# Performance work log

Hardware: AMD Instinct MI355X
Metric: run time of the kernel (lower is better)

The kernel has to match this reference:

```python
import jax, jax.numpy as jnp
import numpy as np

T, B, IN, H, OUT = 128, 128, 512, 512, 512


def _lstm_dir(x, W_ih, W_hh, b_ih, b_hh):
    # x: [T, B, IN]; W_ih: [4H, IN]; W_hh: [4H, H]; biases: [4H]
    # Precompute input contribution for all timesteps in one big GEMM.
    xw = jnp.einsum('tbi,gi->tbg', x, W_ih) + b_ih + b_hh  # [T, B, 4H]
    Hh = W_hh.shape[1]

    def step(carry, xw_t):
        h, c = carry
        gates = xw_t + h @ W_hh.T  # [B, 4H]
        i, f, g, o = jnp.split(gates, 4, axis=-1)  # PyTorch gate order i,f,g,o
        i = jax.nn.sigmoid(i)
        f = jax.nn.sigmoid(f)
        g = jnp.tanh(g)
        o = jax.nn.sigmoid(o)
        c = f * c + i * g
        h = o * jnp.tanh(c)
        return (h, c), h

    h0 = jnp.zeros((x.shape[1], Hh), x.dtype)
    c0 = jnp.zeros((x.shape[1], Hh), x.dtype)
    _, hs = jax.lax.scan(step, (h0, c0), xw)
    return hs  # [T, B, H]


def setup_inputs() -> dict:
    key = jax.random.key(0)
    ks = jax.random.split(key, 12)
    s_in = 1.0 / np.sqrt(H)
    u = lambda k, shape: jax.random.uniform(k, shape, jnp.float32, -s_in, s_in)
    return {
        'x': jax.random.normal(ks[0], (T, B, IN), jnp.float32),
        'W_ih_f': u(ks[1], (4 * H, IN)),
        'W_hh_f': u(ks[2], (4 * H, H)),
        'b_ih_f': u(ks[3], (4 * H,)),
        'b_hh_f': u(ks[4], (4 * H,)),
        'W_ih_b': u(ks[5], (4 * H, IN)),
        'W_hh_b': u(ks[6], (4 * H, H)),
        'b_ih_b': u(ks[7], (4 * H,)),
        'b_hh_b': u(ks[8], (4 * H,)),
        'W_lin': u(ks[9], (OUT, 2 * H)),
        'b_lin': u(ks[10], (OUT,)),
    }


def reference(x, W_ih_f, W_hh_f, b_ih_f, b_hh_f, W_ih_b, W_hh_b, b_ih_b, b_hh_b, W_lin, b_lin):
    h_fwd = _lstm_dir(x, W_ih_f, W_hh_f, b_ih_f, b_hh_f)                    # [T,B,H]
    h_bwd = _lstm_dir(x[::-1], W_ih_b, W_hh_b, b_ih_b, b_hh_b)[::-1]        # [T,B,H]
    out = jnp.concatenate([h_fwd, h_bwd], axis=-1)                          # [T,B,2H]
    out = jnp.einsum('tbh,oh->tbo', out, W_lin) + b_lin                     # [T,B,OUT]
    return out
```

## Files before the change

kernel.cpp:

```cpp
#include <hip/hip_runtime.h>

typedef unsigned short u16;
typedef unsigned long long u64;
typedef __attribute__((ext_vector_type(8))) short bf16x8;
typedef __attribute__((ext_vector_type(4))) float f32x4;

#define MFMA16(a, b, c) __builtin_amdgcn_mfma_f32_16x16x32_bf16((a), (b), (c), 0, 0, 0)

#define TT 128
#define BB 128
#define IN_ 512
#define HH 512
#define G4 2048
#define OUTD 512
#define TB 16384

#define AEXLD(p) __hip_atomic_load((p), __ATOMIC_RELAXED, __HIP_MEMORY_SCOPE_AGENT)

__device__ __forceinline__ u16 f2bf(float f) {
    union { float f; unsigned u; } v; v.f = f;
    unsigned r = v.u + 0x7FFFu + ((v.u >> 16) & 1u);
    return (u16)(r >> 16);
}
__device__ __forceinline__ float bf2f(u16 h) {
    union { unsigned u; float f; } v; v.u = ((unsigned)h) << 16; return v.f;
}
__device__ __forceinline__ float sigmoid_f(float x) { return 1.f / (1.f + __expf(-x)); }
__device__ __forceinline__ float tanh_f(float x) {
    float e = __expf(2.f * x);
    return 1.f - 2.f / (e + 1.f);
}

typedef unsigned __attribute__((address_space(1))) guint;
typedef unsigned __attribute__((address_space(3))) luint;
__device__ __forceinline__ void gll16(const u16* g, u16* l) {
    __builtin_amdgcn_global_load_lds((guint*)(void*)g, (luint*)(void*)l, 16, 0, 0);
}

__global__ void prep_kernel(
    const float* __restrict__ x,
    const float* __restrict__ Wihf, const float* __restrict__ Wihb,
    const float* __restrict__ Whhf, const float* __restrict__ Whhb,
    const float* __restrict__ Wlin,
    const float* __restrict__ bihf, const float* __restrict__ bhhf,
    const float* __restrict__ bihb, const float* __restrict__ bhhb,
    u16* __restrict__ x_bf, u16* __restrict__ wih_cat,
    u16* __restrict__ whhf_bf, u16* __restrict__ whhb_bf,
    u16* __restrict__ wlin_bf, float* __restrict__ bias_cat,
    uint4* __restrict__ exch) {
    const int i0 = blockIdx.x * blockDim.x + threadIdx.x;
    const int stride = gridDim.x * blockDim.x;
    #define CVT4(SRC, DST, N4, DOFF)                                        \
        for (int i = i0; i < (N4); i += stride) {                           \
            float4 v = ((const float4*)(SRC))[i];                           \
            ushort4 o;                                                      \
            o.x = f2bf(v.x); o.y = f2bf(v.y);                               \
            o.z = f2bf(v.z); o.w = f2bf(v.w);                               \
            ((ushort4*)(DST))[(DOFF) + i] = o;                              \
        }
    CVT4(x, x_bf, (TB * IN_) / 4, 0)
    CVT4(Wihf, wih_cat, (G4 * IN_) / 4, 0)
    CVT4(Wihb, wih_cat, (G4 * IN_) / 4, (G4 * IN_) / 4)
    CVT4(Whhf, whhf_bf, (G4 * HH) / 4, 0)
    CVT4(Whhb, whhb_bf, (G4 * HH) / 4, 0)
    CVT4(Wlin, wlin_bf, (OUTD * 2 * HH) / 4, 0)
    #undef CVT4
    for (int i = i0; i < G4; i += stride) {
        bias_cat[i]      = bihf[i] + bhhf[i];
        bias_cat[G4 + i] = bihb[i] + bhhb[i];
    }
    for (int i = i0; i < 65536; i += stride)
        exch[i] = uint4{0u, 0u, 0u, 0u};
}

__global__ __launch_bounds__(256) void gemm_bias_kernel(
    const u16* __restrict__ A, const u16* __restrict__ W,
    const float* __restrict__ bias, void* __restrict__ Cout,
    int M, int N, int K, int out_is_bf16) {
    __shared__ __align__(16) u16 lA[128 * 64];
    __shared__ __align__(16) u16 lB[128 * 64];
    const int tid = threadIdx.x;
    const int m0 = blockIdx.x * 128;
    const int n0 = blockIdx.y * 128;
    const int wave = tid >> 6, lane = tid & 63;
    const int wm = wave >> 1, wn = wave & 1;
    const int lrow = lane & 15, lq = lane >> 4;
    const int srow = lane >> 3, soff = (lane & 7) * 8;

    f32x4 acc[4][4] = {};

    for (int kc = 0; kc < K; kc += 64) {
        #pragma unroll
        for (int i = 0; i < 4; ++i) {
            int chunk = wave + i * 4;
            int row = chunk * 8 + srow;
            gll16(&A[(size_t)(m0 + row) * K + kc + soff], &lA[chunk * 512]);
            gll16(&W[(size_t)(n0 + row) * K + kc + soff], &lB[chunk * 512]);
        }
        __syncthreads();
        #pragma unroll
        for (int ks = 0; ks < 2; ++ks) {
            bf16x8 af[4], bfr[4];
            #pragma unroll
            for (int mf = 0; mf < 4; ++mf)
                af[mf] = *(const bf16x8*)(&lA[(wm * 64 + mf * 16 + lrow) * 64 + ks * 32 + lq * 8]);
            #pragma unroll
            for (int nf = 0; nf < 4; ++nf)
                bfr[nf] = *(const bf16x8*)(&lB[(wn * 64 + nf * 16 + lrow) * 64 + ks * 32 + lq * 8]);
            #pragma unroll
            for (int mf = 0; mf < 4; ++mf)
                #pragma unroll
                for (int nf = 0; nf < 4; ++nf)
                    acc[mf][nf] = MFMA16(af[mf], bfr[nf], acc[mf][nf]);
        }
        __syncthreads();
    }

    #pragma unroll
    for (int mf = 0; mf < 4; ++mf) {
        #pragma unroll
        for (int nf = 0; nf < 4; ++nf) {
            int row = m0 + wm * 64 + mf * 16 + lq * 4;
            int col = n0 + wn * 64 + nf * 16 + lrow;
            float bv = bias[col];
            f32x4 v = acc[mf][nf];
            #pragma unroll
            for (int r = 0; r < 4; ++r) {
                float val = v[r] + bv;
                if (out_is_bf16)
                    ((u16*)Cout)[(size_t)(row + r) * N + col] = f2bf(val);
                else
                    ((float*)Cout)[(size_t)(row + r) * N + col] = val;
            }
        }
    }
}

__global__ __launch_bounds__(256, 1) void lstm_persist_kernel(
    const u16* __restrict__ xw, const u16* __restrict__ whh_f,
    const u16* __restrict__ whh_b, u16* __restrict__ hcat,
    u64* __restrict__ exch) {
    const int bx = blockIdx.x;
    const int dir = bx >> 7;
    const int bt = (bx >> 4) & 7;
    const int jt = bx & 15;
    const u16* __restrict__ whh = dir ? whh_b : whh_f;
    const int b0 = bt * 16;
    const int j0 = jt * 32;

    __shared__ __align__(16) u16 lh[16 * 520];
    __shared__ float sgate[4][16][33];

    const int tid = threadIdx.x;
    const int wave = tid >> 6, lane = tid & 63;
    const int lrow = lane & 15, lq = lane >> 4;

    const u16* wrow = whh + ((size_t)wave * HH + j0) * HH;
    bf16x8 w0[16], w1[16];
    #pragma unroll
    for (int kc = 0; kc < 16; ++kc) {
        w0[kc] = *(const bf16x8*)(&wrow[(size_t)lrow * HH + kc * 32 + lq * 8]);
        w1[kc] = *(const bf16x8*)(&wrow[(size_t)(16 + lrow) * HH + kc * 32 + lq * 8]);
    }
    #pragma unroll
    for (int kc = 0; kc < 16; ++kc)
        asm volatile("" : "+v"(w0[kc]), "+v"(w1[kc]));

    const int bl = tid >> 4;
    const int jj = (tid & 15) * 2;
    float cr0 = 0.f, cr1 = 0.f;

    const size_t my_ex = ((size_t)dir * BB + b0 + bl) * 256 + (j0 >> 1) + (tid & 15);

    for (int s = 0; s < TT; ++s) {
        const int t = dir ? (TT - 1 - s) : s;

        const u16* xrow = xw + ((size_t)t * BB + b0 + bl) * (2 * G4) + dir * G4 + j0 + jj;
        unsigned xg[4];
        #pragma unroll
        for (int g = 0; g < 4; ++g)
            xg[g] = *(const unsigned*)(xrow + (size_t)g * HH);

        f32x4 acc0 = {}, acc1 = {}, acc0b = {}, acc1b = {};
        if (s > 0) {
            const int p = (s - 1) & 1;
            const u64* ex = exch + ((size_t)(p * 2 + dir) * BB + b0) * 256 + tid;
            const u64 expect = ((u64)(unsigned)s << 48) | ((u64)(unsigned)s << 16);
            u64 v[16];
            for (;;) {
                #pragma unroll
                for (int i = 0; i < 16; ++i)
                    v[i] = AEXLD(ex + (size_t)i * 256);
                bool ok = true;
                #pragma unroll
                for (int i = 0; i < 16; ++i)
                    ok &= ((v[i] & 0xFFFF0000FFFF0000ull) == expect);
                if (ok) break;
            }
            #pragma unroll
            for (int i = 0; i < 16; ++i)
                *(unsigned*)(&lh[i * 520 + tid * 2]) =
                    (unsigned)(v[i] & 0xffffu) | (unsigned)((v[i] >> 16) & 0xffff0000u);
            __syncthreads();

            #pragma unroll
            for (int kc = 0; kc < 16; kc += 2) {
                bf16x8 a0 = *(const bf16x8*)(&lh[lrow * 520 + kc * 32 + lq * 8]);
                bf16x8 a1 = *(const bf16x8*)(&lh[lrow * 520 + (kc + 1) * 32 + lq * 8]);
                acc0  = MFMA16(a0, w0[kc], acc0);
                acc1  = MFMA16(a0, w1[kc], acc1);
                acc0b = MFMA16(a1, w0[kc + 1], acc0b);
                acc1b = MFMA16(a1, w1[kc + 1], acc1b);
            }
            acc0 += acc0b;
            acc1 += acc1b;
        }

        #pragma unroll
        for (int r = 0; r < 4; ++r) {
            sgate[wave][lq * 4 + r][lrow]      = acc0[r];
            sgate[wave][lq * 4 + r][16 + lrow] = acc1[r];
        }
        __syncthreads();

        float gi0 = sgate[0][bl][jj]     + bf2f((u16)(xg[0] & 0xffffu));
        float gf0 = sgate[1][bl][jj]     + bf2f((u16)(xg[1] & 0xffffu));
        float gg0 = sgate[2][bl][jj]     + bf2f((u16)(xg[2] & 0xffffu));
        float go0 = sgate[3][bl][jj]     + bf2f((u16)(xg[3] & 0xffffu));
        float gi1 = sgate[0][bl][jj + 1] + bf2f((u16)(xg[0] >> 16));
        float gf1 = sgate[1][bl][jj + 1] + bf2f((u16)(xg[1] >> 16));
        float gg1 = sgate[2][bl][jj + 1] + bf2f((u16)(xg[2] >> 16));
        float go1 = sgate[3][bl][jj + 1] + bf2f((u16)(xg[3] >> 16));

        float c0 = sigmoid_f(gf0) * cr0 + sigmoid_f(gi0) * tanh_f(gg0);
        float c1 = sigmoid_f(gf1) * cr1 + sigmoid_f(gi1) * tanh_f(gg1);
        cr0 = c0; cr1 = c1;
        float h0 = sigmoid_f(go0) * tanh_f(c0);
        float h1 = sigmoid_f(go1) * tanh_f(c1);

        unsigned hb0 = (unsigned)f2bf(h0), hb1 = (unsigned)f2bf(h1);
        unsigned tagv = (unsigned)(s + 1) << 16;
        u64 pv = (u64)(tagv | hb0) | ((u64)(tagv | hb1) << 32);
        __hip_atomic_store(exch + (size_t)((s & 1) * 2) * BB * 256 + my_ex, pv,
                           __ATOMIC_RELAXED, __HIP_MEMORY_SCOPE_AGENT);

        *(unsigned*)(hcat + ((size_t)t * BB + b0 + bl) * (2 * HH) + dir * HH + j0 + jj) =
            hb0 | (hb1 << 16);
    }
}

#define OFF_XBF    ((size_t)0)
#define OFF_WIH    (OFF_XBF  + (size_t)TB * IN_ * 2)
#define OFF_WHHF   (OFF_WIH  + (size_t)2 * G4 * IN_ * 2)
#define OFF_WHHB   (OFF_WHHF + (size_t)G4 * HH * 2)
#define OFF_WLIN   (OFF_WHHB + (size_t)G4 * HH * 2)
#define OFF_BIAS   (OFF_WLIN + (size_t)OUTD * 2 * HH * 2)
#define OFF_XW     (OFF_BIAS + (size_t)2 * G4 * 4)
#define OFF_HCAT   (OFF_XW   + (size_t)TB * 2 * G4 * 2)
#define OFF_EXCH   (OFF_HCAT + (size_t)TB * 2 * HH * 2)
#define WS_NEED    (OFF_EXCH + (size_t)2 * 2 * BB * HH * 4)

extern "C" void kernel_launch(void* const* d_in, const int* in_sizes, int n_in,
                              void* d_out, int out_size, void* d_ws, size_t ws_size,
                              hipStream_t stream) {
    (void)in_sizes; (void)n_in; (void)out_size;
    if (ws_size < WS_NEED) return;

    const float* x    = (const float*)d_in[0];
    const float* Wihf = (const float*)d_in[1];
    const float* Whhf = (const float*)d_in[2];
    const float* bihf = (const float*)d_in[3];
    const float* bhhf = (const float*)d_in[4];
    const float* Wihb = (const float*)d_in[5];
    const float* Whhb = (const float*)d_in[6];
    const float* bihb = (const float*)d_in[7];
    const float* bhhb = (const float*)d_in[8];
    const float* Wlin = (const float*)d_in[9];
    const float* blin = (const float*)d_in[10];
    float* out = (float*)d_out;

    char* ws = (char*)d_ws;
    u16* x_bf     = (u16*)(ws + OFF_XBF);
    u16* wih_cat  = (u16*)(ws + OFF_WIH);
    u16* whhf_bf  = (u16*)(ws + OFF_WHHF);
    u16* whhb_bf  = (u16*)(ws + OFF_WHHB);
    u16* wlin_bf  = (u16*)(ws + OFF_WLIN);
    float* bias_cat = (float*)(ws + OFF_BIAS);
    u16* xw   = (u16*)(ws + OFF_XW);
    u16* hcat = (u16*)(ws + OFF_HCAT);
    u64* exch = (u64*)(ws + OFF_EXCH);

    prep_kernel<<<1024, 256, 0, stream>>>(x, Wihf, Wihb, Whhf, Whhb, Wlin,
                                          bihf, bhhf, bihb, bhhb,
                                          x_bf, wih_cat, whhf_bf, whhb_bf, wlin_bf,
                                          bias_cat, (uint4*)exch);

    gemm_bias_kernel<<<dim3(TB / 128, (2 * G4) / 128), 256, 0, stream>>>(
        x_bf, wih_cat, bias_cat, xw, TB, 2 * G4, IN_, 1);

    {
        void* args[] = { (void*)&xw, (void*)&whhf_bf, (void*)&whhb_bf,
                         (void*)&hcat, (void*)&exch };
        hipError_t e = hipLaunchCooperativeKernel(
            (const void*)lstm_persist_kernel, dim3(256), dim3(256), args, 0, stream);
        if (e != hipSuccess) {
            lstm_persist_kernel<<<256, 256, 0, stream>>>(xw, whhf_bf, whhb_bf,
                                                         hcat, exch);
        }
    }

    gemm_bias_kernel<<<dim3(TB / 128, OUTD / 128), 256, 0, stream>>>(
        hcat, wlin_bf, blin, out, TB, OUTD, 2 * HH, 0);
}
```

Baseline: 693.1 us.

## Fuse input projection GEMM into persistent LSTM kernel with register-resident W_ih

Removes the separate input-projection GEMM and its large bf16 xw buffer. Each persistent block now keeps its slice of W_ih in registers alongside W_hh and computes x_t·W_ih with MFMAs every step, adding the bias in fp32. This cuts a kernel launch and the xw write/read traffic, and removes the bf16 rounding of xw. In exchange it doubles the MFMA work on the sequential critical path and doubles weight register pressure, which risks spills. It also swaps the cooperative launch for a plain launch.

After: 697.6 us. Within noise of the previous version (+0.6%).

```diff
diff --git a/kernel.cpp b/kernel.cpp
--- a/kernel.cpp
+++ b/kernel.cpp
@@ -137,8 +137,9 @@
 }
 
 __global__ __launch_bounds__(256, 1) void lstm_persist_kernel(
-    const u16* __restrict__ xw, const u16* __restrict__ whh_f,
-    const u16* __restrict__ whh_b, u16* __restrict__ hcat,
+    const u16* __restrict__ x_bf, const u16* __restrict__ wih_cat,
+    const u16* __restrict__ whh_f, const u16* __restrict__ whh_b,
+    const float* __restrict__ bias_cat, u16* __restrict__ hcat,
     u64* __restrict__ exch) {
     const int bx = blockIdx.x;
     const int dir = bx >> 7;
@@ -155,31 +156,41 @@
     const int wave = tid >> 6, lane = tid & 63;
     const int lrow = lane & 15, lq = lane >> 4;
 
-    const u16* wrow = whh + ((size_t)wave * HH + j0) * HH;
-    bf16x8 w0[16], w1[16];
+    const u16* wrow_h = whh + ((size_t)wave * HH + j0) * HH;
+    const u16* wrow_x = wih_cat + (size_t)dir * G4 * IN_ + ((size_t)wave * HH + j0) * IN_;
+    bf16x8 w0[16], w1[16], u0[16], u1[16];
     #pragma unroll
     for (int kc = 0; kc < 16; ++kc) {
-        w0[kc] = *(const bf16x8*)(&wrow[(size_t)lrow * HH + kc * 32 + lq * 8]);
-        w1[kc] = *(const bf16x8*)(&wrow[(size_t)(16 + lrow) * HH + kc * 32 + lq * 8]);
+        w0[kc] = *(const bf16x8*)(&wrow_h[(size_t)lrow * HH + kc * 32 + lq * 8]);
+        w1[kc] = *(const bf16x8*)(&wrow_h[(size_t)(16 + lrow) * HH + kc * 32 + lq * 8]);
+        u0[kc] = *(const bf16x8*)(&wrow_x[(size_t)lrow * IN_ + kc * 32 + lq * 8]);
+        u1[kc] = *(const bf16x8*)(&wrow_x[(size_t)(16 + lrow) * IN_ + kc * 32 + lq * 8]);
     }
     #pragma unroll
     for (int kc = 0; kc < 16; ++kc)
-        asm volatile("" : "+v"(w0[kc]), "+v"(w1[kc]));
+        asm volatile("" : "+v"(w0[kc]), "+v"(w1[kc]), "+v"(u0[kc]), "+v"(u1[kc]));
 
     const int bl = tid >> 4;
     const int jj = (tid & 15) * 2;
     float cr0 = 0.f, cr1 = 0.f;
 
+    float bs0[4], bs1[4];
+    #pragma unroll
+    for (int g = 0; g < 4; ++g) {
+        bs0[g] = bias_cat[dir * G4 + g * HH + j0 + jj];
+        bs1[g] = bias_cat[dir * G4 + g * HH + j0 + jj + 1];
+    }
+
     const size_t my_ex = ((size_t)dir * BB + b0 + bl) * 256 + (j0 >> 1) + (tid & 15);
 
     for (int s = 0; s < TT; ++s) {
         const int t = dir ? (TT - 1 - s) : s;
 
-        const u16* xrow = xw + ((size_t)t * BB + b0 + bl) * (2 * G4) + dir * G4 + j0 + jj;
-        unsigned xg[4];
-        #pragma unroll
-        for (int g = 0; g < 4; ++g)
-            xg[g] = *(const unsigned*)(xrow + (size_t)g * HH);
+        const u16* xbase = x_bf + ((size_t)t * BB + b0 + lrow) * IN_ + lq * 8;
+        bf16x8 xf[16];
+        #pragma unroll
+        for (int kc = 0; kc < 16; ++kc)
+            xf[kc] = *(const bf16x8*)(xbase + kc * 32);
 
         f32x4 acc0 = {}, acc1 = {}, acc0b = {}, acc1b = {};
         if (s > 0) {
@@ -205,6 +216,13 @@
 
             #pragma unroll
             for (int kc = 0; kc < 16; kc += 2) {
+                acc0  = MFMA16(xf[kc],     u0[kc],     acc0);
+                acc1  = MFMA16(xf[kc],     u1[kc],     acc1);
+                acc0b = MFMA16(xf[kc + 1], u0[kc + 1], acc0b);
+                acc1b = MFMA16(xf[kc + 1], u1[kc + 1], acc1b);
+            }
+            #pragma unroll
+            for (int kc = 0; kc < 16; kc += 2) {
                 bf16x8 a0 = *(const bf16x8*)(&lh[lrow * 520 + kc * 32 + lq * 8]);
                 bf16x8 a1 = *(const bf16x8*)(&lh[lrow * 520 + (kc + 1) * 32 + lq * 8]);
                 acc0  = MFMA16(a0, w0[kc], acc0);
@@ -214,6 +232,16 @@
             }
             acc0 += acc0b;
             acc1 += acc1b;
+        } else {
+            #pragma unroll
+            for (int kc = 0; kc < 16; kc += 2) {
+                acc0  = MFMA16(xf[kc],     u0[kc],     acc0);
+                acc1  = MFMA16(xf[kc],     u1[kc],     acc1);
+                acc0b = MFMA16(xf[kc + 1], u0[kc + 1], acc0b);
+                acc1b = MFMA16(xf[kc + 1], u1[kc + 1], acc1b);
+            }
+            acc0 += acc0b;
+            acc1 += acc1b;
         }
 
         #pragma unroll
@@ -223,14 +251,14 @@
         }
         __syncthreads();
 
-        float gi0 = sgate[0][bl][jj]     + bf2f((u16)(xg[0] & 0xffffu));
-        float gf0 = sgate[1][bl][jj]     + bf2f((u16)(xg[1] & 0xffffu));
-        float gg0 = sgate[2][bl][jj]     + bf2f((u16)(xg[2] & 0xffffu));
-        float go0 = sgate[3][bl][jj]     + bf2f((u16)(xg[3] & 0xffffu));
-        float gi1 = sgate[0][bl][jj + 1] + bf2f((u16)(xg[0] >> 16));
-        float gf1 = sgate[1][bl][jj + 1] + bf2f((u16)(xg[1] >> 16));
-        float gg1 = sgate[2][bl][jj + 1] + bf2f((u16)(xg[2] >> 16));
-        float go1 = sgate[3][bl][jj + 1] + bf2f((u16)(xg[3] >> 16));
+        float gi0 = sgate[0][bl][jj]     + bs0[0];
+        float gf0 = sgate[1][bl][jj]     + bs0[1];
+        float gg0 = sgate[2][bl][jj]     + bs0[2];
+        float go0 = sgate[3][bl][jj]     + bs0[3];
+        float gi1 = sgate[0][bl][jj + 1] + bs1[0];
+        float gf1 = sgate[1][bl][jj + 1] + bs1[1];
+        float gg1 = sgate[2][bl][jj + 1] + bs1[2];
+        float go1 = sgate[3][bl][jj + 1] + bs1[3];
 
         float c0 = sigmoid_f(gf0) * cr0 + sigmoid_f(gi0) * tanh_f(gg0);
         float c1 = sigmoid_f(gf1) * cr1 + sigmoid_f(gi1) * tanh_f(gg1);
@@ -255,8 +283,7 @@
 #define OFF_WHHB   (OFF_WHHF + (size_t)G4 * HH * 2)
 #define OFF_WLIN   (OFF_WHHB + (size_t)G4 * HH * 2)
 #define OFF_BIAS   (OFF_WLIN + (size_t)OUTD * 2 * HH * 2)
-#define OFF_XW     (OFF_BIAS + (size_t)2 * G4 * 4)
-#define OFF_HCAT   (OFF_XW   + (size_t)TB * 2 * G4 * 2)
+#define OFF_HCAT   (OFF_BIAS + (size_t)2 * G4 * 4)
 #define OFF_EXCH   (OFF_HCAT + (size_t)TB * 2 * HH * 2)
 #define WS_NEED    (OFF_EXCH + (size_t)2 * 2 * BB * HH * 4)
 
@@ -286,7 +313,6 @@
     u16* whhb_bf  = (u16*)(ws + OFF_WHHB);
     u16* wlin_bf  = (u16*)(ws + OFF_WLIN);
     float* bias_cat = (float*)(ws + OFF_BIAS);
-    u16* xw   = (u16*)(ws + OFF_XW);
     u16* hcat = (u16*)(ws + OFF_HCAT);
     u64* exch = (u64*)(ws + OFF_EXCH);
 
@@ -295,19 +321,8 @@
                                           x_bf, wih_cat, whhf_bf, whhb_bf, wlin_bf,
                                           bias_cat, (uint4*)exch);
 
-    gemm_bias_kernel<<<dim3(TB / 128, (2 * G4) / 128), 256, 0, stream>>>(
-        x_bf, wih_cat, bias_cat, xw, TB, 2 * G4, IN_, 1);
-
-    {
-        void* args[] = { (void*)&xw, (void*)&whhf_bf, (void*)&whhb_bf,
-                         (void*)&hcat, (void*)&exch };
-        hipError_t e = hipLaunchCooperativeKernel(
-            (const void*)lstm_persist_kernel, dim3(256), dim3(256), args, 0, stream);
-        if (e != hipSuccess) {
-            lstm_persist_kernel<<<256, 256, 0, stream>>>(xw, whhf_bf, whhb_bf,
-                                                         hcat, exch);
-        }
-    }
+    lstm_persist_kernel<<<256, 256, 0, stream>>>(x_bf, wih_cat, whhf_bf, whhb_bf,
+                                                 bias_cat, hcat, exch);
 
     gemm_bias_kernel<<<dim3(TB / 128, OUTD / 128), 256, 0, stream>>>(
         hcat, wlin_bf, blin, out, TB, OUTD, 2 * HH, 0);
```
